# Kernel tuning notes

Measured on AMD Instinct MI355X. Metric: run time of the kernel, lower is better.

Reference implementation:

```python
import jax, jax.numpy as jnp
import numpy as np

D_MODEL = 1024
NUM_HEADS = 16
HEAD_DIM = D_MODEL // NUM_HEADS  # 64
N = 1024
B = 8


def setup_inputs() -> dict:
    key = jax.random.key(0)
    ks = jax.random.split(key, 11)
    s = 0.02
    inp = {
        'query': jax.random.normal(ks[0], (B, D_MODEL, N), jnp.float32),
        'key':   jax.random.normal(ks[1], (B, D_MODEL, N), jnp.float32),
        'value': jax.random.normal(ks[2], (B, D_MODEL, N), jnp.float32),
        # 1x1 conv1d == linear over channel dim: weight [out, in], bias [out]
        'Wq': jax.random.normal(ks[3], (D_MODEL, D_MODEL), jnp.float32) * s,
        'bq': jax.random.normal(ks[4], (D_MODEL,), jnp.float32) * s,
        'Wk': jax.random.normal(ks[5], (D_MODEL, D_MODEL), jnp.float32) * s,
        'bk': jax.random.normal(ks[6], (D_MODEL,), jnp.float32) * s,
        'Wv': jax.random.normal(ks[7], (D_MODEL, D_MODEL), jnp.float32) * s,
        'bv': jax.random.normal(ks[8], (D_MODEL,), jnp.float32) * s,
        'Wm': jax.random.normal(ks[9], (D_MODEL, D_MODEL), jnp.float32) * s,
        'bm': jax.random.normal(ks[10], (D_MODEL,), jnp.float32) * s,
    }
    return inp


def _proj(W, b, x):
    # nn.Conv1d(kernel_size=1): out[b,o,n] = sum_i W[o,i] x[b,i,n] + b[o]
    return jnp.einsum('oi,bin->bon', W, x) + b[None, :, None]


def reference(query, key, value, Wq, bq, Wk, bk, Wv, bv, Wm, bm):
    Bd = query.shape[0]
    # view(B, dim, heads, N): channel axis split as (head_dim, num_heads)
    q = _proj(Wq, bq, query).reshape(Bd, HEAD_DIM, NUM_HEADS, -1)
    k = _proj(Wk, bk, key).reshape(Bd, HEAD_DIM, NUM_HEADS, -1)
    v = _proj(Wv, bv, value).reshape(Bd, HEAD_DIM, NUM_HEADS, -1)
    scale = 1.0 / (HEAD_DIM ** 0.5)
    scores = jnp.einsum('bdhn,bdhm->bhnm', q, k) * scale  # [B,H,N,N]
    prob = jax.nn.softmax(scores, axis=-1)
    x = jnp.einsum('bhnm,bdhm->bdhn', prob, v)  # [B,D,H,N]
    out = _proj(Wm, bm, x.reshape(Bd, HEAD_DIM * NUM_HEADS, -1))
    return out
```

## Files before the change

### kernel.cpp

```cpp
#include <hip/hip_runtime.h>

typedef __bf16 bf16x8 __attribute__((ext_vector_type(8)));
typedef __bf16 bf16x4 __attribute__((ext_vector_type(4)));
typedef float f32x4 __attribute__((ext_vector_type(4)));
typedef unsigned short u16;
typedef unsigned int u32;

__device__ __forceinline__ u16 f2bf(float f) {
  u32 u = __builtin_bit_cast(u32, f);
  u = (u + 0x7FFFu + ((u >> 16) & 1u)) >> 16;
  return (u16)u;
}

__device__ __forceinline__ void gload_lds16(const void* g, void* l) {
  __builtin_amdgcn_global_load_lds((const __attribute__((address_space(1))) void*)g,
                                   (__attribute__((address_space(3))) void*)l, 16, 0, 0);
}

__global__ __launch_bounds__(256) void transpose_cast3(const float* __restrict__ q,
                                                       const float* __restrict__ k,
                                                       const float* __restrict__ v,
                                                       u16* __restrict__ X3) {
  __shared__ float T[64][68];
  int tid = threadIdx.x;
  int n0 = blockIdx.x * 64, i0 = blockIdx.y * 64;
  int z = blockIdx.z;
  int which = z >> 3, b = z & 7;
  const float* src = (which == 0) ? q : (which == 1) ? k : v;
  size_t boff = (size_t)b << 20;
  const float* s = src + boff;
  u16* d = X3 + ((size_t)which << 23) + boff;
  int ir = tid >> 4, n4 = (tid & 15) * 4;
#pragma unroll
  for (int r = 0; r < 4; ++r) {
    int i_loc = ir + r * 16;
    float4 vv = *(const float4*)(s + (size_t)(i0 + i_loc) * 1024 + n0 + n4);
    *(float4*)&T[i_loc][n4] = vv;
  }
  __syncthreads();
  int nr = tid >> 3, i8 = (tid & 7) * 8;
#pragma unroll
  for (int r = 0; r < 2; ++r) {
    int n_loc = nr + r * 32;
    u32 pk[4];
#pragma unroll
    for (int j = 0; j < 4; ++j) {
      float f0 = T[i8 + 2 * j][n_loc];
      float f1 = T[i8 + 2 * j + 1][n_loc];
      pk[j] = (u32)f2bf(f0) | ((u32)f2bf(f1) << 16);
    }
    *(uint4*)(d + (size_t)(n0 + n_loc) * 1024 + i0 + i8) = make_uint4(pk[0], pk[1], pk[2], pk[3]);
  }
}

__global__ __launch_bounds__(256) void transpose_cast(const float* __restrict__ src,
                                                      u16* __restrict__ dst) {
  __shared__ float T[64][68];
  int tid = threadIdx.x;
  int n0 = blockIdx.x * 64, i0 = blockIdx.y * 64;
  size_t boff = (size_t)blockIdx.z << 20;
  const float* s = src + boff;
  u16* d = dst + boff;
  int ir = tid >> 4, n4 = (tid & 15) * 4;
#pragma unroll
  for (int r = 0; r < 4; ++r) {
    int i_loc = ir + r * 16;
    float4 v = *(const float4*)(s + (size_t)(i0 + i_loc) * 1024 + n0 + n4);
    *(float4*)&T[i_loc][n4] = v;
  }
  __syncthreads();
  int nr = tid >> 3, i8 = (tid & 7) * 8;
#pragma unroll
  for (int r = 0; r < 2; ++r) {
    int n_loc = nr + r * 32;
    u32 pk[4];
#pragma unroll
    for (int j = 0; j < 4; ++j) {
      float f0 = T[i8 + 2 * j][n_loc];
      float f1 = T[i8 + 2 * j + 1][n_loc];
      pk[j] = (u32)f2bf(f0) | ((u32)f2bf(f1) << 16);
    }
    *(uint4*)(d + (size_t)(n0 + n_loc) * 1024 + i0 + i8) = make_uint4(pk[0], pk[1], pk[2], pk[3]);
  }
}

__global__ __launch_bounds__(256) void cast_weights(const float* __restrict__ Wq,
                                                    const float* __restrict__ Wk,
                                                    const float* __restrict__ Wv,
                                                    const float* __restrict__ Wm,
                                                    u16* __restrict__ out) {
  int w = blockIdx.y;
  const float* src = (w == 0) ? Wq : (w == 1) ? Wk : (w == 2) ? Wv : Wm;
  u16* dst = out + ((size_t)w << 20);
  int o = blockIdx.x;
  int c4 = threadIdx.x * 4;
  float f[4];
  if (w < 3) {
    float4 v = *(const float4*)(src + (size_t)o * 1024 + c4);
    f[0] = v.x; f[1] = v.y; f[2] = v.z; f[3] = v.w;
  } else {
#pragma unroll
    for (int j = 0; j < 4; ++j) {
      int cp = c4 + j;
      f[j] = src[(size_t)o * 1024 + (cp & 63) * 16 + (cp >> 6)];
    }
  }
  u32 p0 = (u32)f2bf(f[0]) | ((u32)f2bf(f[1]) << 16);
  u32 p1 = (u32)f2bf(f[2]) | ((u32)f2bf(f[3]) << 16);
  *(uint2*)(dst + (size_t)o * 1024 + c4) = make_uint2(p0, p1);
}

__device__ __forceinline__ void gemm_body(const u16* __restrict__ A,
                                          const u16* __restrict__ B,
                                          const float* __restrict__ bias,
                                          void* __restrict__ Out, float escale,
                                          int epi, u16* LD) {
  int tid = threadIdx.x;
  int wave = tid >> 6, l = tid & 63, ln = l & 15, g = l >> 4;
  int wm = wave >> 2, wn = wave & 3;
  int bid = blockIdx.x;
  int mt = (bid >> 3) & 7;
  int nt = ((bid & 7) << 2) | (bid >> 6);
  int c0 = mt * 128, n0 = nt * 256;

  int R = tid >> 3, sl = tid & 7;
  int v = sl ^ (R & 7);
  int sa = v >> 2, sg = v & 3;
  const u16* aSrc = A + (size_t)(c0 + 2 * R + sa) * 1024 + sg * 8;
  const u16* bSrc0 = B + (size_t)(n0 + 2 * R + sa) * 1024 + sg * 8;
  const u16* bSrc1 = B + (size_t)(n0 + 128 + 2 * R + sa) * 1024 + sg * 8;

  int slr = ((((ln & 1) << 2) | g) ^ ((ln >> 1) & 7)) * 8;
  int laneA = (wm * 32 + (ln >> 1)) * 64 + slr;
  int laneB = (wn * 32 + (ln >> 1)) * 64 + slr;

  f32x4 acc[4][4] = {};

#define STAGE(buf, kt)                                                   \
  do {                                                                   \
    gload_lds16(aSrc + (kt) * 32, &LD[(buf) * 4096 + tid * 8]);          \
    gload_lds16(bSrc0 + (kt) * 32, &LD[16384 + (buf) * 8192 + tid * 8]); \
    gload_lds16(bSrc1 + (kt) * 32,                                       \
                &LD[16384 + (buf) * 8192 + 4096 + tid * 8]);             \
  } while (0)

  STAGE(0, 0);
  STAGE(1, 1);
  STAGE(2, 2);

#pragma unroll
  for (int t = 0; t < 32; ++t) {
    if (t < 30)
      asm volatile("s_waitcnt vmcnt(6)" ::: "memory");
    else if (t == 30)
      asm volatile("s_waitcnt vmcnt(3)" ::: "memory");
    else
      asm volatile("s_waitcnt vmcnt(0)" ::: "memory");
    asm volatile("s_barrier" ::: "memory");
    if (t <= 28) STAGE((t + 3) & 3, t + 3);
    const int ab = (t & 3) * 4096;
    const int bb = 16384 + (t & 3) * 8192;
    bf16x8 af[4], bfr[4];
#pragma unroll
    for (int mm = 0; mm < 4; ++mm) af[mm] = *(const bf16x8*)&LD[ab + laneA + mm * 512];
#pragma unroll
    for (int nn = 0; nn < 4; ++nn) bfr[nn] = *(const bf16x8*)&LD[bb + laneB + nn * 512];
    __builtin_amdgcn_s_setprio(1);
#pragma unroll
    for (int mm = 0; mm < 4; ++mm)
#pragma unroll
      for (int nn = 0; nn < 4; ++nn)
        acc[mm][nn] = __builtin_amdgcn_mfma_f32_16x16x32_bf16(af[mm], bfr[nn], acc[mm][nn], 0, 0, 0);
    __builtin_amdgcn_s_setprio(0);
  }
#undef STAGE

  int D0 = (c0 >> 4) + wm * 4;
#pragma unroll
  for (int nn = 0; nn < 4; ++nn) {
    size_t ng = (size_t)n0 + wn * 64 + nn * 16 + ln;
#pragma unroll
    for (int r = 0; r < 4; ++r) {
      int h = g * 4 + r;
      if (epi == 0) {
        bf16x4 pk;
#pragma unroll
        for (int mm = 0; mm < 4; ++mm) {
          int c = c0 + wm * 64 + mm * 16 + h;
          pk[mm] = (__bf16)((acc[mm][nn][r] + bias[c]) * escale);
        }
        *(bf16x4*)((u16*)Out + ng * 1024 + (size_t)h * 64 + D0) = pk;
      } else {
        size_t b = ng >> 10, n = ng & 1023;
#pragma unroll
        for (int mm = 0; mm < 4; ++mm) {
          int c = c0 + wm * 64 + mm * 16 + h;
          float val = (acc[mm][nn][r] + bias[c]) * escale;
          if (epi == 1) {
            int d = D0 + mm;
            ((u16*)Out)[((b * 16 + h) * 64 + d) * 1024 + n] = f2bf(val);
          } else {
            ((float*)Out)[(b << 20) + (size_t)c * 1024 + n] = val;
          }
        }
      }
    }
  }
}

template <int EPI>
__global__ __launch_bounds__(512, 2) void gemm4b(const u16* __restrict__ A,
                                                 const u16* __restrict__ B,
                                                 const float* __restrict__ bias,
                                                 void* __restrict__ Out, float escale) {
  __shared__ u16 LD[49152];
  gemm_body(A, B, bias, Out, escale, EPI, LD);
}

__global__ __launch_bounds__(512, 2) void gemm_qkv(const u16* __restrict__ Wbf,
                                                   const u16* __restrict__ X3,
                                                   const float* __restrict__ bq,
                                                   const float* __restrict__ bk,
                                                   const float* __restrict__ bv,
                                                   u16* __restrict__ Qh,
                                                   u16* __restrict__ Kh,
                                                   u16* __restrict__ Vt, float qscale) {
  __shared__ u16 LD[49152];
  int z = blockIdx.y;
  const u16* A = Wbf + ((size_t)z << 20);
  const u16* B = X3 + ((size_t)z << 23);
  const float* bias = (z == 0) ? bq : (z == 1) ? bk : bv;
  void* Out = (z == 0) ? (void*)Qh : (z == 1) ? (void*)Kh : (void*)Vt;
  float escale = (z == 0) ? qscale : 1.0f;
  int epi = (z == 2) ? 1 : 0;
  gemm_body(A, B, bias, Out, escale, epi, LD);
}

__global__ __launch_bounds__(256) void attn_kernel(const u16* __restrict__ Qh,
                                                   const u16* __restrict__ Kh,
                                                   const u16* __restrict__ Vt,
                                                   u16* __restrict__ Xh) {
  __shared__ u16 Ks[2][4096];
  __shared__ u16 Vs[2][4096];
  __shared__ u16 Ps[8][16 * 72];
  int tid = threadIdx.x;
  int w = tid >> 6, l = tid & 63, ln = l & 15, g = l >> 4;
  int id = blockIdx.x;
  int qp = (id & 63) >> 3;
  int bh = ((id >> 6) << 3) | (id & 7);
  size_t b = bh >> 4;
  int h = bh & 15;
  const u16* Qg = Qh + (b << 20) + (h << 6);
  const u16* Kg = Kh + (b << 20) + (h << 6);
  const u16* Vg = Vt + ((size_t)bh << 16);
  u16* Og = Xh + (b << 20) + (h << 6);

  bf16x8 qf[2][2];
#pragma unroll
  for (int t = 0; t < 2; ++t)
#pragma unroll
    for (int kk = 0; kk < 2; ++kk)
      qf[t][kk] = *(const bf16x8*)(Qg + (size_t)(qp * 128 + t * 64 + w * 16 + ln) * 1024 + kk * 32 + g * 8);

  int lr = l >> 3;
  int sw8 = ((l & 7) ^ lr) << 3;
  int r0 = w * 16 + lr, r1 = r0 + 8;
  const u16* kS0 = Kg + (size_t)r0 * 1024 + sw8;
  const u16* kS1 = Kg + (size_t)r1 * 1024 + sw8;
  const u16* vS0 = Vg + (size_t)r0 * 1024 + sw8;
  const u16* vS1 = Vg + (size_t)r1 * 1024 + sw8;

  f32x4 xacc[2][4] = {};
  float lacc[2] = {0.f, 0.f};

  gload_lds16(kS0, &Ks[0][(w * 2) * 512]);
  gload_lds16(kS1, &Ks[0][(w * 2 + 1) * 512]);
  gload_lds16(vS0, &Vs[0][(w * 2) * 512]);
  gload_lds16(vS1, &Vs[0][(w * 2 + 1) * 512]);
  __syncthreads();

  int sx = ln & 7;
  int cur = 0;
  for (int kt = 0; kt < 16; ++kt) {
    if (kt < 15) {
      int nxt = cur ^ 1;
      gload_lds16(kS0 + (size_t)(kt + 1) * 65536, &Ks[nxt][(w * 2) * 512]);
      gload_lds16(kS1 + (size_t)(kt + 1) * 65536, &Ks[nxt][(w * 2 + 1) * 512]);
      gload_lds16(vS0 + (kt + 1) * 64, &Vs[nxt][(w * 2) * 512]);
      gload_lds16(vS1 + (kt + 1) * 64, &Vs[nxt][(w * 2 + 1) * 512]);
    }
    bf16x8 kf[2][4], vf[2][4];
#pragma unroll
    for (int kk = 0; kk < 2; ++kk)
#pragma unroll
      for (int f = 0; f < 4; ++f) {
        int slot = (((kk << 2) + g) ^ sx) << 3;
        kf[kk][f] = *(const bf16x8*)&Ks[cur][(f * 16 + ln) * 64 + slot];
        vf[kk][f] = *(const bf16x8*)&Vs[cur][(f * 16 + ln) * 64 + slot];
      }
    f32x4 sacc[2][4] = {};
#pragma unroll
    for (int t = 0; t < 2; ++t)
#pragma unroll
      for (int kk = 0; kk < 2; ++kk)
#pragma unroll
        for (int f = 0; f < 4; ++f)
          sacc[t][f] = __builtin_amdgcn_mfma_f32_16x16x32_bf16(kf[kk][f], qf[t][kk], sacc[t][f], 0, 0, 0);
#pragma unroll
    for (int t = 0; t < 2; ++t) {
      u16* PsW = Ps[w * 2 + t];
#pragma unroll
      for (int f = 0; f < 4; ++f) {
        float p0 = __builtin_amdgcn_exp2f(sacc[t][f][0]);
        float p1 = __builtin_amdgcn_exp2f(sacc[t][f][1]);
        float p2 = __builtin_amdgcn_exp2f(sacc[t][f][2]);
        float p3 = __builtin_amdgcn_exp2f(sacc[t][f][3]);
        lacc[t] += (p0 + p1) + (p2 + p3);
        bf16x4 pb;
        pb[0] = (__bf16)p0; pb[1] = (__bf16)p1; pb[2] = (__bf16)p2; pb[3] = (__bf16)p3;
        *(bf16x4*)&PsW[ln * 72 + (f << 4) + (g << 2)] = pb;
      }
    }
#pragma unroll
    for (int t = 0; t < 2; ++t) {
      const u16* PsR = Ps[w * 2 + t];
#pragma unroll
      for (int kk = 0; kk < 2; ++kk) {
        bf16x8 pf = *(const bf16x8*)&PsR[ln * 72 + (kk << 5) + (g << 3)];
#pragma unroll
        for (int fd = 0; fd < 4; ++fd)
          xacc[t][fd] = __builtin_amdgcn_mfma_f32_16x16x32_bf16(pf, vf[kk][fd], xacc[t][fd], 0, 0, 0);
      }
    }
    __syncthreads();
    cur ^= 1;
  }

#pragma unroll
  for (int t = 0; t < 2; ++t) {
    float lt = lacc[t];
    lt += __shfl_xor(lt, 16);
    lt += __shfl_xor(lt, 32);
    float il[4];
#pragma unroll
    for (int r = 0; r < 4; ++r) il[r] = 1.0f / __shfl(lt, g * 4 + r);
#pragma unroll
    for (int fd = 0; fd < 4; ++fd)
#pragma unroll
      for (int r = 0; r < 4; ++r) {
        int nq = qp * 128 + t * 64 + w * 16 + g * 4 + r;
        Og[(size_t)nq * 1024 + fd * 16 + ln] = f2bf(xacc[t][fd][r] * il[r]);
      }
  }
}

extern "C" void kernel_launch(void* const* d_in, const int* in_sizes, int n_in,
                              void* d_out, int out_size, void* d_ws, size_t ws_size,
                              hipStream_t stream) {
  const float* q  = (const float*)d_in[0];
  const float* k  = (const float*)d_in[1];
  const float* v  = (const float*)d_in[2];
  const float* Wq = (const float*)d_in[3];
  const float* bq = (const float*)d_in[4];
  const float* Wk = (const float*)d_in[5];
  const float* bk = (const float*)d_in[6];
  const float* Wv = (const float*)d_in[7];
  const float* bv = (const float*)d_in[8];
  const float* Wm = (const float*)d_in[9];
  const float* bm = (const float*)d_in[10];

  char* ws = (char*)d_ws;
  u16* Wbf = (u16*)ws;
  u16* Qh  = (u16*)(ws + (8ull << 20));
  u16* Kh  = (u16*)(ws + (24ull << 20));
  u16* Vt  = (u16*)(ws + (40ull << 20));
  u16* X3  = (u16*)(ws + (56ull << 20));

  cast_weights<<<dim3(1024, 4, 1), 256, 0, stream>>>(Wq, Wk, Wv, Wm, Wbf);

  const float qscale = 0.125f * 1.44269504088896340736f;

  if (ws_size >= (104ull << 20)) {
    transpose_cast3<<<dim3(16, 16, 24), 256, 0, stream>>>(q, k, v, X3);
    gemm_qkv<<<dim3(256, 3), 512, 0, stream>>>(Wbf, X3, bq, bk, bv, Qh, Kh, Vt, qscale);
  } else {
    dim3 tg(16, 16, 8);
    transpose_cast<<<tg, 256, 0, stream>>>(q, X3);
    gemm4b<0><<<256, 512, 0, stream>>>(Wbf, X3, bq, Qh, qscale);
    transpose_cast<<<tg, 256, 0, stream>>>(k, X3);
    gemm4b<0><<<256, 512, 0, stream>>>(Wbf + (1u << 20), X3, bk, Kh, 1.0f);
    transpose_cast<<<tg, 256, 0, stream>>>(v, X3);
    gemm4b<1><<<256, 512, 0, stream>>>(Wbf + (2u << 20), X3, bv, Vt, 1.0f);
  }

  attn_kernel<<<1024, 256, 0, stream>>>(Qh, Kh, Vt, X3);

  gemm4b<2><<<256, 512, 0, stream>>>(Wbf + (3u << 20), X3, bm, d_out, 1.0f);
}
```

Measured before the change: 185.6 us.

## Keep softmax probabilities in registers by permuting V fragment k-order

Removes the LDS round trip for the probability tile. The exp2'd scores are now packed directly into bf16x8 MFMA A-operands, and V fragments are loaded as two bf16x4 halves so their k-ordering matches the register layout of the score accumulator. This eliminates the per-wave P staging buffer, its writes and reads, and frees LDS. It also adds a launch-bounds occupancy hint of 4 blocks per SM, at the cost of twice as many, narrower V LDS reads.

```diff
diff --git a/kernel.cpp b/kernel.cpp
--- a/kernel.cpp
+++ b/kernel.cpp
@@ -5,6 +5,8 @@
 typedef float f32x4 __attribute__((ext_vector_type(4)));
 typedef unsigned short u16;
 typedef unsigned int u32;
+
+typedef union { bf16x8 v8; bf16x4 v4[2]; } bfu;
 
 __device__ __forceinline__ u16 f2bf(float f) {
   u32 u = __builtin_bit_cast(u32, f);
@@ -236,13 +238,12 @@
   gemm_body(A, B, bias, Out, escale, epi, LD);
 }
 
-__global__ __launch_bounds__(256) void attn_kernel(const u16* __restrict__ Qh,
-                                                   const u16* __restrict__ Kh,
-                                                   const u16* __restrict__ Vt,
-                                                   u16* __restrict__ Xh) {
+__global__ __launch_bounds__(256, 4) void attn_kernel(const u16* __restrict__ Qh,
+                                                      const u16* __restrict__ Kh,
+                                                      const u16* __restrict__ Vt,
+                                                      u16* __restrict__ Xh) {
   __shared__ u16 Ks[2][4096];
   __shared__ u16 Vs[2][4096];
-  __shared__ u16 Ps[8][16 * 72];
   int tid = threadIdx.x;
   int w = tid >> 6, l = tid & 63, ln = l & 15, g = l >> 4;
   int id = blockIdx.x;
@@ -289,15 +290,28 @@
       gload_lds16(vS0 + (kt + 1) * 64, &Vs[nxt][(w * 2) * 512]);
       gload_lds16(vS1 + (kt + 1) * 64, &Vs[nxt][(w * 2 + 1) * 512]);
     }
-    bf16x8 kf[2][4], vf[2][4];
+    bf16x8 kf[2][4];
 #pragma unroll
     for (int kk = 0; kk < 2; ++kk)
 #pragma unroll
       for (int f = 0; f < 4; ++f) {
         int slot = (((kk << 2) + g) ^ sx) << 3;
         kf[kk][f] = *(const bf16x8*)&Ks[cur][(f * 16 + ln) * 64 + slot];
-        vf[kk][f] = *(const bf16x8*)&Vs[cur][(f * 16 + ln) * 64 + slot];
       }
+    bf16x8 vf[2][4];
+#pragma unroll
+    for (int kk = 0; kk < 2; ++kk) {
+      int s0 = (kk << 2) + (g >> 1);
+      int off = (g & 1) << 2;
+#pragma unroll
+      for (int fd = 0; fd < 4; ++fd) {
+        int rowb = (fd * 16 + ln) * 64;
+        bfu uv;
+        uv.v4[0] = *(const bf16x4*)&Vs[cur][rowb + ((s0 ^ sx) << 3) + off];
+        uv.v4[1] = *(const bf16x4*)&Vs[cur][rowb + (((s0 + 2) ^ sx) << 3) + off];
+        vf[kk][fd] = uv.v8;
+      }
+    }
     f32x4 sacc[2][4] = {};
 #pragma unroll
     for (int t = 0; t < 2; ++t)
@@ -308,29 +322,29 @@
           sacc[t][f] = __builtin_amdgcn_mfma_f32_16x16x32_bf16(kf[kk][f], qf[t][kk], sacc[t][f], 0, 0, 0);
 #pragma unroll
     for (int t = 0; t < 2; ++t) {
-      u16* PsW = Ps[w * 2 + t];
-#pragma unroll
-      for (int f = 0; f < 4; ++f) {
-        float p0 = __builtin_amdgcn_exp2f(sacc[t][f][0]);
-        float p1 = __builtin_amdgcn_exp2f(sacc[t][f][1]);
-        float p2 = __builtin_amdgcn_exp2f(sacc[t][f][2]);
-        float p3 = __builtin_amdgcn_exp2f(sacc[t][f][3]);
-        lacc[t] += (p0 + p1) + (p2 + p3);
-        bf16x4 pb;
-        pb[0] = (__bf16)p0; pb[1] = (__bf16)p1; pb[2] = (__bf16)p2; pb[3] = (__bf16)p3;
-        *(bf16x4*)&PsW[ln * 72 + (f << 4) + (g << 2)] = pb;
+      bf16x8 pf[2];
+#pragma unroll
+      for (int kk = 0; kk < 2; ++kk) {
+        bfu up;
+#pragma unroll
+        for (int e2 = 0; e2 < 2; ++e2) {
+          int f = 2 * kk + e2;
+          float p0 = __builtin_amdgcn_exp2f(sacc[t][f][0]);
+          float p1 = __builtin_amdgcn_exp2f(sacc[t][f][1]);
+          float p2 = __builtin_amdgcn_exp2f(sacc[t][f][2]);
+          float p3 = __builtin_amdgcn_exp2f(sacc[t][f][3]);
+          lacc[t] += (p0 + p1) + (p2 + p3);
+          bf16x4 pb;
+          pb[0] = (__bf16)p0; pb[1] = (__bf16)p1; pb[2] = (__bf16)p2; pb[3] = (__bf16)p3;
+          up.v4[e2] = pb;
+        }
+        pf[kk] = up.v8;
       }
-    }
-#pragma unroll
-    for (int t = 0; t < 2; ++t) {
-      const u16* PsR = Ps[w * 2 + t];
-#pragma unroll
-      for (int kk = 0; kk < 2; ++kk) {
-        bf16x8 pf = *(const bf16x8*)&PsR[ln * 72 + (kk << 5) + (g << 3)];
+#pragma unroll
+      for (int kk = 0; kk < 2; ++kk)
 #pragma unroll
         for (int fd = 0; fd < 4; ++fd)
-          xacc[t][fd] = __builtin_amdgcn_mfma_f32_16x16x32_bf16(pf, vf[kk][fd], xacc[t][fd], 0, 0, 0);
-      }
+          xacc[t][fd] = __builtin_amdgcn_mfma_f32_16x16x32_bf16(pf[kk], vf[kk][fd], xacc[t][fd], 0, 0, 0);
     }
     __syncthreads();
     cur ^= 1;
```

Result: faster. 180.8 us (-2.6%).
